# Kernel optimization log

Hardware: AMD Instinct MI355X
Metric: run time of the kernel (lower is better)

## Reference

```python
import jax, jax.numpy as jnp
import numpy as np

EPS = 1e-5


def _vfe(x, w, b, g, beta):
    # x: (B, Nv, Np, Cin) -> (B, Nv, Cout). Linear -> BatchNorm1d(train stats) -> ReLU -> max over points.
    y = jnp.einsum('bnpc,oc->bnpo', x, w) + b
    mu = y.mean(axis=(0, 1, 2))
    var = y.var(axis=(0, 1, 2))  # biased, as used by torch BN normalization
    y = (y - mu) * jax.lax.rsqrt(var + EPS) * g + beta
    y = jax.nn.relu(y)
    return y.max(axis=2)


def _conv_bn_relu(x, w, b, g, beta):
    # x: (B, Cin, D, H, W); w: (Cout, Cin, 3, 3, 3); stride 2, padding 1.
    y = jax.lax.conv_general_dilated(x, w, (2, 2, 2), [(1, 1)] * 3,
                                     dimension_numbers=('NCDHW', 'OIDHW', 'NCDHW'))
    y = y + b[None, :, None, None, None]
    mu = y.mean(axis=(0, 2, 3, 4), keepdims=True)
    var = y.var(axis=(0, 2, 3, 4), keepdims=True)
    y = (y - mu) * jax.lax.rsqrt(var + EPS) * g[None, :, None, None, None] + beta[None, :, None, None, None]
    return jax.nn.relu(y)


def setup_inputs() -> dict:
    key = jax.random.key(0)
    ks = jax.random.split(key, 16)
    B, Nv, Np, Cin = 2, 12000, 32, 5
    VF = 128  # voxel_feat_dim
    OUT = 256  # output_feat_dim
    D, H, W = 20, 128, 128
    s = 0.05
    inp = {
        'voxel_features': jax.random.normal(ks[0], (B, Nv, Np, Cin), jnp.float32),
        'voxel_coords': jax.random.randint(ks[1], (B, Nv, 3), 0, 20, jnp.int32),
        'D': D, 'H': H, 'W': W,
        # VFE1: 5 -> 64
        'w1': jax.random.normal(ks[2], (VF // 2, Cin), jnp.float32) * s,
        'b1': jnp.zeros((VF // 2,), jnp.float32),
        'g1': jnp.ones((VF // 2,), jnp.float32),
        'be1': jnp.zeros((VF // 2,), jnp.float32),
        # VFE2: 64 -> 128
        'w2': jax.random.normal(ks[3], (VF, VF // 2), jnp.float32) * s,
        'b2': jnp.zeros((VF,), jnp.float32),
        'g2': jnp.ones((VF,), jnp.float32),
        'be2': jnp.zeros((VF,), jnp.float32),
        # conv3d_1: 128 -> 128
        'cw1': jax.random.normal(ks[4], (128, VF, 3, 3, 3), jnp.float32) * s,
        'cb1': jnp.zeros((128,), jnp.float32),
        'cg1': jnp.ones((128,), jnp.float32),
        'cbe1': jnp.zeros((128,), jnp.float32),
        # conv3d_2: 128 -> 256
        'cw2': jax.random.normal(ks[5], (256, 128, 3, 3, 3), jnp.float32) * s,
        'cb2': jnp.zeros((256,), jnp.float32),
        'cg2': jnp.ones((256,), jnp.float32),
        'cbe2': jnp.zeros((256,), jnp.float32),
        # conv3d_3: 256 -> 256
        'cw3': jax.random.normal(ks[6], (OUT, 256, 3, 3, 3), jnp.float32) * s,
        'cb3': jnp.zeros((OUT,), jnp.float32),
        'cg3': jnp.ones((OUT,), jnp.float32),
        'cbe3': jnp.zeros((OUT,), jnp.float32),
    }
    return inp


def reference(voxel_features, voxel_coords, D, H, W,
              w1, b1, g1, be1, w2, b2, g2, be2,
              cw1, cb1, cg1, cbe1, cw2, cb2, cg2, cbe2, cw3, cb3, cg3, cbe3):
    # VFE stages
    f = _vfe(voxel_features, w1, b1, g1, be1)   # (B, Nv, 64)
    f = _vfe(f[:, :, None, :] * 1.0 if False else f.reshape(f.shape[0], f.shape[1], 1, -1), w2, b2, g2, be2) if False else None
    # proper: vfe2 operates on (B, Nv, Np, C) but after vfe1 features are (B, Nv, C);
    # torch code passes 3D tensor? No: vfe2 receives (B, Nv, 64) reshaped -- actually torch
    # VFELayer expects 4D; original forward feeds (B, Nv, 64) which unpacks as (B, Nv, 64)->error-free
    # only if treated as (B, Nv, Np=64, C)? We match the documented intent: treat vfe1 output as
    # (B, Nv, 1, 64) so vfe2's max over points is a no-op.
    f1 = _vfe(voxel_features, w1, b1, g1, be1)          # (B, Nv, 64)
    f2 = _vfe(f1[:, :, None, :], w2, b2, g2, be2)       # (B, Nv, 128)
    B, Nv, C = f2.shape
    # scatter voxel features into dense grid (B, C, D, H, W)
    def scat(feat, coords):
        grid = jnp.zeros((C, D, H, W), feat.dtype)
        return grid.at[:, coords[:, 0], coords[:, 1], coords[:, 2]].set(feat.T)
    grid = jax.vmap(scat)(f2, voxel_coords)
    x = _conv_bn_relu(grid, cw1, cb1, cg1, cbe1)
    x = _conv_bn_relu(x, cw2, cb2, cg2, cbe2)
    x = _conv_bn_relu(x, cw3, cb3, cg3, cbe3)
    return x
```

## Files before the change

kernel.cpp:

```cpp
#include <hip/hip_runtime.h>
#include <hip/hip_bf16.h>

#define EPS 1e-5f

#define BB 2
#define NV 12000
#define NP 32
#define CIN 5
#define GD 20

typedef __attribute__((ext_vector_type(8))) short bf16x8;
typedef __attribute__((ext_vector_type(4))) float f32x4;

static const size_t OFF_SX   = 0;
static const size_t OFF_MST  = 32;
static const size_t OFF_AC1  = 4192;
static const size_t OFF_AC2  = 4320;
static const size_t OFF_ACB1 = 4576;
static const size_t OFF_ACB2 = 4960;
static const size_t OFF_AC3  = 7520;
static const size_t OFF_BG2  = 8032;
static const size_t OFF_BG3  = 10080;
static const size_t OFF_W2T  = 13152;
static const size_t OFF_WIN  = 21344;
static const size_t OFF_F1   = 37344;
static const size_t OFF_I0CL = 1573344;
static const size_t OFF_I1   = 3059168;
static const size_t OFF_I2   = 3644896;
static const size_t OFF_WT1B = 4031968;
static const size_t OFF_WT2  = 4253152;
static const size_t OFF_WT3  = 5137888;
static const size_t OFF_RAW1 = 6907360;
static const size_t OFF_RAW2 = 8146400;
static const size_t OFF_RAW3 = 9620960;
static const size_t OFF_MSTP = 10407392;
static const size_t OFF_SXP  = 11472352;

__global__ __launch_bounds__(256) void k_front(const float* __restrict__ cw2, const float* __restrict__ cw3,
                                               const float* __restrict__ w2, const float* __restrict__ cw1,
                                               float* __restrict__ wT2, float* __restrict__ wT3,
                                               float* __restrict__ w2T, __hip_bfloat16* __restrict__ wT1b,
                                               float* __restrict__ I0z, float* __restrict__ bgz,
                                               int* __restrict__ winp,
                                               const float* __restrict__ vf, float* __restrict__ sxp,
                                               const float* __restrict__ w1,
                                               float* __restrict__ mxb, float* __restrict__ mnb){
    __shared__ float shm[5200];
    int blk = blockIdx.x;
    int t = threadIdx.x;
    if (blk >= 1892){
        int wave = t >> 6, lane = t & 63;
        int v = (blk - 1892)*4 + wave;
        float w[5];
        #pragma unroll
        for (int c=0;c<5;c++) w[c] = w1[lane*5+c];
        const float* x = vf + (size_t)v*(NP*CIN);
        float mx = -1e30f, mn = 1e30f;
        #pragma unroll
        for (int pc = 0; pc < 8; pc++) {
            float xx[20];
            const float4* x4 = (const float4*)(x + pc*20);
            #pragma unroll
            for (int i=0;i<5;i++){ float4 q = x4[i]; xx[4*i]=q.x; xx[4*i+1]=q.y; xx[4*i+2]=q.z; xx[4*i+3]=q.w; }
            #pragma unroll
            for (int j=0;j<4;j++){
                float y = xx[j*5]*w[0]+xx[j*5+1]*w[1]+xx[j*5+2]*w[2]+xx[j*5+3]*w[3]+xx[j*5+4]*w[4];
                mx = fmaxf(mx, y); mn = fminf(mn, y);
            }
        }
        mxb[(size_t)v*64 + lane] = mx;
        mnb[(size_t)v*64 + lane] = mn;
        return;
    }
    if (blk >= 1142){
        int sb = blk - 1142;
        float* st = shm; float* sw = shm + 5120;
        const float4* src = (const float4*)(vf + (size_t)sb*5120);
        #pragma unroll
        for (int i=0;i<5;i++) ((float4*)st)[i*256 + t] = src[i*256 + t];
        __syncthreads();
        float vals[20];
        #pragma unroll
        for (int i=0;i<20;i++) vals[i]=0.f;
        const float* base = st + t*20;
        #pragma unroll
        for (int p=0;p<4;p++){
            const float* v2 = base + p*5;
            int k=5;
            #pragma unroll
            for (int c=0;c<5;c++){
                vals[c]+=v2[c];
                #pragma unroll
                for(int c2=c;c2<5;c2++){ vals[k++]+=v2[c]*v2[c2]; }
            }
        }
        #pragma unroll
        for (int off=32; off>0; off>>=1){
            #pragma unroll
            for (int i=0;i<20;i++) vals[i] += __shfl_down(vals[i], off);
        }
        int wave = t>>6, lane = t&63;
        if (lane==0){
            #pragma unroll
            for (int i=0;i<20;i++) sw[wave*20+i]=vals[i];
        }
        __syncthreads();
        if (t<20){
            float s = sw[t]+sw[20+t]+sw[40+t]+sw[60+t];
            sxp[(size_t)t*768 + sb] = s;
        }
        return;
    }
    if (blk >= 1141){
        int4* d = (int4*)winp;
        int4 mone; mone.x=-1; mone.y=-1; mone.z=-1; mone.w=-1;
        #pragma unroll
        for (int k=0;k<16;k++){
            int idx = k*256 + t;
            if (idx < 4000) d[idx] = mone;
        }
        return;
    }
    if (blk == 1140){
        float4 z; z.x=0.f; z.y=0.f; z.z=0.f; z.w=0.f;
        float4* d = (float4*)bgz;
        #pragma unroll
        for (int k=0;k<5;k++) d[k*256 + t] = z;
        return;
    }
    if (blk >= 777){
        float4 z; z.x=0.f; z.y=0.f; z.z=0.f; z.w=0.f;
        float4* d = (float4*)I0z;
        int base = (blk - 777)*1024;
        #pragma unroll
        for (int k=0;k<4;k++){
            int idx = base + k*256 + t;
            if (idx < 371456) d[idx] = z;
        }
        return;
    }
    if (blk >= 649){
        int co = blk - 649;
        float* tlw = shm;
        for (int j=t; j<3456; j+=256) tlw[j] = cw1[(size_t)co*3456 + j];
        __syncthreads();
        for (int idx=t; idx<3456; idx+=256){
            int tap = idx >> 7, ci = idx & 127;
            wT1b[((size_t)(tap*128 + co) << 7) + ci] = __float2bfloat16(tlw[ci*27 + tap]);
        }
        return;
    }
    if (blk == 648){
        for (int i=t; i<8192; i+=256){ int o=i>>6, c=i&63; w2T[c*128+o]=w2[i]; }
        return;
    }
    const float* src; float* dst; int CO, R;
    if (blk < 216){ src=cw2; dst=wT2; CO=256; R=3456; }
    else { blk-=216; src=cw3; dst=wT3; CO=256; R=6912; }
    int nrt = R/64;
    int rt = blk % nrt, ct = blk / nrt;
    int r0 = rt*64, c0 = ct*64;
    float (*tl)[65] = (float(*)[65])shm;
    int tj = threadIdx.x & 63;
    int ti0 = threadIdx.x >> 6;
    #pragma unroll
    for (int k=0;k<16;k++){
        int i = ti0 + k*4;
        tl[i][tj] = src[(size_t)(c0+i)*R + r0 + tj];
    }
    __syncthreads();
    #pragma unroll
    for (int k=0;k<16;k++){
        int j = ti0 + k*4;
        dst[(size_t)(r0+j)*CO + c0 + tj] = tl[tj][j];
    }
}

__global__ __launch_bounds__(256) void k_red_sx_ac1(const float* __restrict__ sxp,
                                                    const float* __restrict__ w1, const float* __restrict__ b1,
                                                    const float* __restrict__ g1, const float* __restrict__ be1,
                                                    float* __restrict__ AC1,
                                                    const int* __restrict__ coords, int* __restrict__ winner){
    if (blockIdx.x >= 1){
        int i = (blockIdx.x - 1)*256 + threadIdx.x;
        if (i >= BB*NV) return;
        int b = i / NV, n = i % NV;
        int d = coords[(size_t)i*3], h = coords[(size_t)i*3+1], w = coords[(size_t)i*3+2];
        if (d<0||d>=GD||h<0||h>=GD||w<0||w>=GD) return;
        atomicMax(&winner[b*8000 + d*400 + h*20 + w], n);
        return;
    }
    __shared__ float S[20];
    int t = threadIdx.x;
    int wave = t>>6, lane = t&63;
    for (int c = wave; c < 20; c += 4){
        float s = 0.f;
        for (int b = lane; b < 750; b += 64) s += sxp[(size_t)c*768 + b];
        #pragma unroll
        for (int off=32; off>0; off>>=1) s += __shfl_down(s, off);
        if (lane==0) S[c] = s;
    }
    __syncthreads();
    int o = t; if (o>=64) return;
    const float N = (float)(BB*NV*NP);
    float w[5];
    #pragma unroll
    for(int c=0;c<5;c++) w[c]=w1[o*5+c];
    float b=b1[o];
    float wd=0;
    #pragma unroll
    for(int c=0;c<5;c++) wd += w[c]*S[c];
    float m = wd/N + b;
    float q=0; int kk=5;
    for(int c=0;c<5;c++) for(int c2=c;c2<5;c2++){ float s=S[kk++]; q += (c==c2?1.f:2.f)*w[c]*w[c2]*s; }
    q = q/N + 2.f*b*wd/N + b*b;
    float var = q - m*m;
    float A = g1[o]*rsqrtf(var + EPS);
    AC1[o] = A;
    AC1[64+o] = be1[o] + (b - m)*A;
}

__global__ __launch_bounds__(256) void k_stats_f1p(const float* __restrict__ mxb, const float* __restrict__ mnb,
                                                   const float* __restrict__ AC1,
                                                   float* __restrict__ f1, float* __restrict__ Mpart){
    __shared__ float Ash[64], Csh[64];
    __shared__ float tile[16][64];
    __shared__ float ssum[64];
    int t = threadIdx.x;
    if (t < 64){ Ash[t]=AC1[t]; Csh[t]=AC1[64+t]; ssum[t]=0.f; }
    float acc[4][4];
    #pragma unroll
    for(int i=0;i<4;i++)
        #pragma unroll
        for(int j=0;j<4;j++) acc[i][j]=0.f;
    int i4 = (t>>4)*4, j4 = (t&15)*4;
    const int NT = (BB*NV)/16;
    for (int tl = blockIdx.x; tl < NT; tl += gridDim.x) {
        __syncthreads();
        for (int i = t; i < 16*64; i += 256){
            int o = i & 63;
            float a = Ash[o];
            float vmx = mxb[(size_t)tl*1024 + i];
            float vmn = mnb[(size_t)tl*1024 + i];
            float f = fmaxf(a*((a>=0.f)?vmx:vmn) + Csh[o], 0.f);
            tile[i>>6][o] = f;
            f1[(size_t)tl*1024 + i] = f;
        }
        __syncthreads();
        #pragma unroll
        for (int r=0;r<16;r++){
            float a[4], bb[4];
            #pragma unroll
            for (int u=0;u<4;u++) a[u]=tile[r][i4+u];
            #pragma unroll
            for (int u=0;u<4;u++) bb[u]=tile[r][j4+u];
            #pragma unroll
            for (int u=0;u<4;u++)
                #pragma unroll
                for (int q=0;q<4;q++) acc[u][q] += a[u]*bb[q];
        }
        if (t < 64) {
            float s=0;
            #pragma unroll
            for(int r=0;r<16;r++) s+=tile[r][t];
            ssum[t]+=s;
        }
    }
    float* mp = Mpart + (size_t)blockIdx.x*4160;
    #pragma unroll
    for(int i=0;i<4;i++)
        #pragma unroll
        for(int j=0;j<4;j++) mp[(size_t)(i4+i)*64 + (j4+j)] = acc[i][j];
    __syncthreads();
    if (t<64) mp[4096 + t] = ssum[t];
}

__global__ __launch_bounds__(64) void k_red_mst(const float* __restrict__ Mpart, float* __restrict__ Mst){
    int e = blockIdx.x*64 + threadIdx.x;
    if (e >= 4160) return;
    float s = 0.f;
    #pragma unroll 8
    for (int p=0;p<256;p++) s += Mpart[(size_t)p*4160 + e];
    Mst[e] = s;
}

__global__ __launch_bounds__(64) void k_ac2(const float* __restrict__ Mst, const float* __restrict__ w2,
                                            const float* __restrict__ b2, const float* __restrict__ g2,
                                            const float* __restrict__ be2, float* __restrict__ AC2){
    int o = blockIdx.x;
    int j = threadIdx.x;
    const float N = (float)(BB*NV);
    const float* M = Mst; const float* sv = Mst+4096;
    const float* wrow = w2 + o*64;
    float wj = wrow[j];
    float sj = 0.f;
    #pragma unroll 8
    for (int c=0;c<64;c++) sj += wrow[c]*M[c*64+j];
    float q = wj*sj;
    float wdp = wj*sv[j];
    #pragma unroll
    for (int off=32; off>0; off>>=1){ q += __shfl_down(q,off); wdp += __shfl_down(wdp,off); }
    if (j==0){
        float b = b2[o];
        float m = wdp/N + b;
        float qq = q/N + 2.f*b*wdp/N + b*b;
        float var = qq - m*m;
        float A = g2[o]*rsqrtf(var+EPS);
        AC2[o]=A; AC2[128+o]= be2[o] + (b-m)*A;
    }
}


__global__ __launch_bounds__(256) void k_I0(const int* __restrict__ winner, const float* __restrict__ f1,
                                            const float* __restrict__ w2T, const float* __restrict__ AC2,
                                            __hip_bfloat16* __restrict__ I0cl){
    int blk = blockIdx.x;
    int b = blk / 400; int dh = blk % 400;
    int d = dh / 20, h = dh % 20;
    __shared__ int win[20];
    __shared__ float f1sh[20][64];
    __shared__ float sh[20*128];
    int t = threadIdx.x;
    if (t < 20) win[t] = winner[b*8000 + dh*20 + t];
    __syncthreads();
    for (int idx = t; idx < 1280; idx += 256){
        int cell = idx >> 6, c = idx & 63;
        int n = win[cell];
        f1sh[cell][c] = (n>=0) ? f1[((size_t)(b*NV+n))*64 + c] : 0.f;
    }
    __syncthreads();
    int o = t & 127;
    int half = t >> 7;
    float A = AC2[o], C = AC2[128+o];
    float wreg[64];
    #pragma unroll
    for (int c=0;c<64;c++) wreg[c] = w2T[c*128+o];
    for (int p=0;p<10;p++){
        int cell = p*2 + half;
        float acc = 0.f;
        if (win[cell] >= 0){
            #pragma unroll
            for (int c=0;c<64;c++) acc += f1sh[cell][c]*wreg[c];
            acc = fmaxf(acc*A + C, 0.f);
        }
        sh[cell*128 + o] = acc;
    }
    __syncthreads();
    __hip_bfloat16* outp = I0cl + (((size_t)(b*21 + d+1)*23 + h+1)*24 + 1)*128;
    for (int idx = t; idx < 2560; idx += 256) outp[idx] = __float2bfloat16(sh[idx]);
}

__global__ __launch_bounds__(256) void k_conv1m(const __hip_bfloat16* __restrict__ I0cl,
                                                const __hip_bfloat16* __restrict__ wT1b,
                                                float* __restrict__ raw1){
    int blk = blockIdx.x;
    int oh = blk % 11; int r2 = blk / 11;
    int od = r2 % 10; int b = r2 / 10;
    __shared__ float4 ldsv[3456];
    char* lds = (char*)ldsv;
    int t = threadIdx.x;
    for (int i = t; i < 3456; i += 256){
        int row = i >> 4;
        int dh = row / 24, w = row % 24;
        int dd = dh / 3, hh = dh % 3;
        const char* src = (const char*)(I0cl + (((size_t)(b*21 + 2*od+dd)*23 + 2*oh+hh)*24 + w)*128);
        float4 v = *(const float4*)(src + (i & 15)*16);
        int lb = i*16;
        *(float4*)(lds + (lb ^ ((row & 7) << 4))) = v;
    }
    __syncthreads();
    int wave = t >> 6, lane = t & 63;
    int col = lane & 15, quad = lane >> 4;
    int co0 = wave*32;
    f32x4 acc0 = {0.f,0.f,0.f,0.f};
    f32x4 acc1 = {0.f,0.f,0.f,0.f};
    for (int kd=0; kd<3; kd++){
        for (int kh=0; kh<3; kh++){
            #pragma unroll
            for (int kw=0; kw<3; kw++){
                int tap = (kd*3+kh)*3 + kw;
                int wi = 2*col + kw; if (wi > 23) wi = 23;
                int row = (kd*3+kh)*24 + wi;
                int lbbase = (row << 8) + quad*16;
                int xr = (row & 7) << 4;
                const __hip_bfloat16* ap0 = wT1b + (size_t)tap*16384 + (co0 + col)*128 + quad*8;
                #pragma unroll
                for (int q=0; q<4; q++){
                    bf16x8 b0 = *(const bf16x8*)(lds + ((lbbase + q*64) ^ xr));
                    bf16x8 a0 = *(const bf16x8*)(ap0 + q*32);
                    bf16x8 a1 = *(const bf16x8*)(ap0 + q*32 + 2048);
                    acc0 = __builtin_amdgcn_mfma_f32_16x16x32_bf16(a0, b0, acc0, 0, 0, 0);
                    acc1 = __builtin_amdgcn_mfma_f32_16x16x32_bf16(a1, b0, acc1, 0, 0, 0);
                }
            }
        }
    }
    if (col < 11){
        #pragma unroll
        for (int r=0;r<4;r++){
            int co = co0 + quad*4 + r;
            raw1[(((size_t)(b*128+co)*10 + od)*11 + oh)*11 + col] = acc0[r];
        }
        #pragma unroll
        for (int r=0;r<4;r++){
            int co = co0 + 16 + quad*4 + r;
            raw1[(((size_t)(b*128+co)*10 + od)*11 + oh)*11 + col] = acc1[r];
        }
    }
}

__global__ __launch_bounds__(256) void k_stats_c1(const float* __restrict__ raw1, const float* __restrict__ cb,
                                                  const float* __restrict__ cg, const float* __restrict__ cbe,
                                                  float* __restrict__ ACb1){
    int co = blockIdx.x;
    float s=0, ss=0;
    for (int b=0;b<2;b++){
        size_t base = ((size_t)(b*128+co))*1210;
        for (int i=threadIdx.x; i<1210; i+=256){
            float v = raw1[base+i];
            s+=v; ss+=v*v;
        }
    }
    __shared__ float sh1[256], sh2[256];
    sh1[threadIdx.x]=s; sh2[threadIdx.x]=ss; __syncthreads();
    for (int st=128; st>0; st>>=1){
        if (threadIdx.x<st){ sh1[threadIdx.x]+=sh1[threadIdx.x+st]; sh2[threadIdx.x]+=sh2[threadIdx.x+st]; }
        __syncthreads();
    }
    if (threadIdx.x==0){
        float bias = cb[co];
        const float N = 81920.f;
        float sum_y = sh1[0] + N*bias;
        float ssq_y = sh2[0] + 2.f*bias*sh1[0] + N*bias*bias;
        float m = sum_y/N;
        float var = ssq_y/N - m*m;
        float A = cg[co]*rsqrtf(var+EPS);
        float C = cbe[co] - m*A;
        ACb1[co]=A; ACb1[128+co]=C;
        ACb1[256+co]=fmaxf(bias*A + C, 0.f);
    }
}

__global__ __launch_bounds__(256) void k_fill_I1_bg2(const float* __restrict__ raw1, const float* __restrict__ ACb1,
                                                     const float* __restrict__ cb, float* __restrict__ I1p,
                                                     const float* __restrict__ cw2, float* __restrict__ bgraw2){
    if (blockIdx.x >= 2288){
        int o = blockIdx.x - 2288;
        int t = threadIdx.x;
        float acc[8];
        #pragma unroll
        for (int c=0;c<8;c++) acc[c]=0.f;
        if (t < 128){
            int ci = t;
            float w[27];
            const float* wp = cw2 + (size_t)o*3456 + ci*27;
            #pragma unroll
            for (int k=0;k<27;k++) w[k] = wp[k];
            float bg = ACb1[256+ci];
            float sw0[9], sw1[9];
            #pragma unroll
            for (int t9=0;t9<9;t9++){ sw1[t9]=w[3*t9+1]+w[3*t9+2]; sw0[t9]=w[3*t9]+sw1[t9]; }
            #pragma unroll
            for (int cls=0; cls<8; cls++){
                const int d0=(cls>>2)&1, h0=(cls>>1)&1, w0=cls&1;
                float ws=0.f;
                #pragma unroll
                for (int kd=0;kd<3;kd++){
                    if (d0 && kd==0) continue;
                    #pragma unroll
                    for (int kh=0;kh<3;kh++){
                        if (h0 && kh==0) continue;
                        ws += w0 ? sw1[kd*3+kh] : sw0[kd*3+kh];
                    }
                }
                acc[cls] = bg*ws;
            }
        }
        #pragma unroll
        for (int off=32; off>0; off>>=1){
            #pragma unroll
            for (int c=0;c<8;c++) acc[c] += __shfl_down(acc[c], off);
        }
        __shared__ float sred[4][8];
        if ((t&63)==0){
            #pragma unroll
            for (int c=0;c<8;c++) sred[t>>6][c] = acc[c];
        }
        __syncthreads();
        if (t < 8) bgraw2[o*8+t] = sred[0][t]+sred[1][t]+sred[2][t]+sred[3][t];
        return;
    }
    int i = blockIdx.x*blockDim.x + threadIdx.x;
    int wpad = i % 16; int r = i / 16;
    int hpad = r % 13; r /= 13;
    int dpad = r % 11; r /= 11;
    int ci = r % 128; int b = r / 128;
    float val;
    if (dpad==0 || hpad==0 || wpad==0 || wpad>12) val = 0.f;
    else {
        int d = dpad-1, h = hpad-1, w = wpad-1;
        if (h < 11 && w < 11){
            size_t idx = (((size_t)(b*128+ci)*10 + d)*11 + h)*11 + w;
            val = fmaxf((raw1[idx] + cb[ci])*ACb1[ci] + ACb1[128+ci], 0.f);
        } else val = ACb1[256+ci];
    }
    I1p[i] = val;
}

__global__ __launch_bounds__(256) void k_conv2(const float* __restrict__ I1p, const float* __restrict__ wT2,
                                               float* __restrict__ raw2){
    int blk = blockIdx.x;
    int ciq = blk & 15; blk >>= 4;
    int oh = blk % 6; blk /= 6;
    int od = blk % 5; int b = blk / 5;
    int wave = threadIdx.x >> 6, lane = threadIdx.x & 63;
    float acc[4][6];
    #pragma unroll
    for (int q=0;q<4;q++)
        #pragma unroll
        for (int i=0;i<6;i++) acc[q][i]=0.f;
    int ci0 = ciq*8 + wave*2;
    for (int ci = ci0; ci < ci0+2; ci++){
        const float* base = I1p + ((size_t)(b*128+ci)*11 + 2*od)*208 + (2*oh)*16;
        const float* wp0 = wT2 + (size_t)ci*27*256 + lane;
        #pragma unroll
        for (int kd=0;kd<3;kd++){
            #pragma unroll
            for (int kh=0;kh<3;kh++){
                float row[16];
                const float4* rp = (const float4*)(base + kd*208 + kh*16);
                #pragma unroll
                for (int i=0;i<4;i++){ float4 t=rp[i]; row[4*i]=t.x; row[4*i+1]=t.y; row[4*i+2]=t.z; row[4*i+3]=t.w; }
                const float* wp = wp0 + (kd*3+kh)*3*256;
                #pragma unroll
                for (int kw=0;kw<3;kw++){
                    float w0=wp[kw*256], w1=wp[kw*256+64], w2v=wp[kw*256+128], w3=wp[kw*256+192];
                    #pragma unroll
                    for (int ow=0;ow<6;ow++){
                        float x = row[2*ow+kw];
                        acc[0][ow]+=x*w0; acc[1][ow]+=x*w1; acc[2][ow]+=x*w2v; acc[3][ow]+=x*w3;
                    }
                }
            }
        }
    }
    __shared__ float red[4*1540];
    #pragma unroll
    for (int q=0;q<4;q++)
        #pragma unroll
        for (int ow=0;ow<6;ow++) red[wave*1540 + lane*24 + q*6 + ow] = acc[q][ow];
    __syncthreads();
    float* rb = raw2 + (size_t)ciq*92160;
    for (int idx = threadIdx.x; idx < 1536; idx += 256){
        int lane2 = idx/24, j = idx%24;
        float s = red[0*1540 + lane2*24 + j] + red[1*1540 + lane2*24 + j]
                + red[2*1540 + lane2*24 + j] + red[3*1540 + lane2*24 + j];
        int q = j/6, ow = j%6;
        int co = q*64 + lane2;
        rb[(((size_t)(b*256+co)*5 + od)*6 + oh)*6 + ow] = s;
    }
}

__global__ __launch_bounds__(64) void k_stats_c2(const float* __restrict__ raw2, const float* __restrict__ bgraw2,
                                                 const float* __restrict__ cb2, const float* __restrict__ cg2,
                                                 const float* __restrict__ cbe2, float* __restrict__ ACb2){
    int o = blockIdx.x;
    int lane = threadIdx.x;
    float s=0.f, ss=0.f;
    for (int idx=lane; idx<360; idx+=64){
        int b = idx/180; int p = idx%180;
        int d = p/36; int rem = p%36; int h = rem/6; int w = rem%6;
        size_t base = (((size_t)(b*256+o)*5 + d)*6 + h)*6 + w;
        float v = 0.f;
        #pragma unroll
        for (int q=0;q<16;q++) v += raw2[q*92160+base];
        s += v; ss += v*v;
    }
    #pragma unroll
    for (int off=32; off>0; off>>=1){ s += __shfl_down(s,off); ss += __shfl_down(ss,off); }
    if (lane==0){
        const int n2[8] = {3744,104,104,0,936,26,26,0};
        float bgv[8];
        #pragma unroll
        for (int c=0;c<8;c++){ bgv[c]=bgraw2[o*8+c]; s += 2.f*n2[c]*bgv[c]; ss += 2.f*n2[c]*bgv[c]*bgv[c]; }
        const float N = 10240.f;
        float b = cb2[o];
        float sum_y = s + N*b;
        float ssq_y = ss + 2.f*b*s + N*b*b;
        float m = sum_y/N;
        float var = ssq_y/N - m*m;
        float A = cg2[o]*rsqrtf(var+EPS); float C = cbe2[o] - m*A;
        ACb2[o]=A; ACb2[256+o]=C;
        for (int c=0;c<8;c++) ACb2[512+o*8+c] = fmaxf((bgv[c]+b)*A + C, 0.f);
    }
}

__global__ __launch_bounds__(256) void k_fill_I2_bg3(const float* __restrict__ raw2, const float* __restrict__ ACb2,
                                                     const float* __restrict__ cb2, float* __restrict__ I2p,
                                                     const float* __restrict__ cw3, float* __restrict__ bgraw3){
    if (blockIdx.x >= 1512){
        int o = blockIdx.x - 1512;
        int t = threadIdx.x;
        float sum12[12];
        {
            int ci = t;
            float w[27];
            const float* wp = cw3 + ((size_t)o*256 + ci)*27;
            #pragma unroll
            for (int k=0;k<27;k++) w[k] = wp[k];
            const float* bg = ACb2 + 512 + ci*8;
            float bgv[8];
            #pragma unroll
            for (int q=0;q<8;q++) bgv[q]=bg[q];
            #pragma unroll
            for (int c=0;c<12;c++){
                const int odc = c>>2; const int h0 = (c>>1)&1; const int w0 = c&1;
                float sum = 0.f;
                #pragma unroll
                for (int kd=0;kd<3;kd++){
                    const int d = 2*odc-1+kd; if (d<0||d>=5) continue;
                    const int db = (d==0)?4:0;
                    #pragma unroll
                    for (int kh=0;kh<3;kh++){
                        if (h0 && kh==0) continue;
                        const int hb = (h0 && kh==1)?2:0;
                        #pragma unroll
                        for (int kw=0;kw<3;kw++){
                            if (w0 && kw==0) continue;
                            const int wb = (w0 && kw==1)?1:0;
                            sum += bgv[db|hb|wb]*w[(kd*3+kh)*3+kw];
                        }
                    }
                }
                sum12[c] = sum;
            }
        }
        #pragma unroll
        for (int off=32; off>0; off>>=1){
            #pragma unroll
            for (int c=0;c<12;c++) sum12[c] += __shfl_down(sum12[c], off);
        }
        __shared__ float sred[4][12];
        if ((t&63)==0){
            #pragma unroll
            for (int c=0;c<12;c++) sred[t>>6][c] = sum12[c];
        }
        __syncthreads();
        if (t < 12) bgraw3[o*12+t] = sred[0][t]+sred[1][t]+sred[2][t]+sred[3][t];
        return;
    }
    int i = blockIdx.x*blockDim.x + threadIdx.x;
    int wpad = i % 12; int r = i / 12;
    int hpad = r % 9; r /= 9;
    int dpad = r % 7; r /= 7;
    int ci = r % 256; int b = r / 256;
    float val;
    if (dpad==0 || dpad==6 || hpad==0 || wpad==0 || wpad>8) val = 0.f;
    else {
        int d = dpad-1, h = hpad-1, w = wpad-1;
        if (h<6 && w<6){
            size_t idx = (((size_t)(b*256+ci)*5 + d)*6 + h)*6 + w;
            float raw = 0.f;
            #pragma unroll
            for (int q=0;q<16;q++) raw += raw2[q*92160+idx];
            val = fmaxf((raw + cb2[ci])*ACb2[ci] + ACb2[256+ci], 0.f);
        } else {
            int cls = ((d==0)?4:0) | ((h==0)?2:0) | ((w==0)?1:0);
            val = ACb2[512 + ci*8 + cls];
        }
    }
    I2p[i] = val;
}

__global__ __launch_bounds__(256) void k_conv3(const float* __restrict__ I2p, const float* __restrict__ wT3,
                                               float* __restrict__ raw3){
    int blk = blockIdx.x;
    int ciq = blk & 31; blk >>= 5;
    int oh = blk % 4; blk /= 4;
    int od = blk % 3; int b = blk / 3;
    int wave = threadIdx.x >> 6, lane = threadIdx.x & 63;
    float acc[4][4];
    #pragma unroll
    for (int q=0;q<4;q++)
        #pragma unroll
        for (int i=0;i<4;i++) acc[q][i]=0.f;
    int ci0 = ciq*8 + wave*2;
    for (int ci = ci0; ci < ci0+2; ci++){
        const float* base = I2p + ((size_t)(b*256+ci)*7 + 2*od)*108 + (2*oh)*12;
        const float* wp0 = wT3 + (size_t)ci*27*256 + lane;
        #pragma unroll
        for (int kd=0;kd<3;kd++){
            #pragma unroll
            for (int kh=0;kh<3;kh++){
                float row[12];
                const float4* rp = (const float4*)(base + kd*108 + kh*12);
                #pragma unroll
                for (int i=0;i<3;i++){ float4 t=rp[i]; row[4*i]=t.x; row[4*i+1]=t.y; row[4*i+2]=t.z; row[4*i+3]=t.w; }
                const float* wp = wp0 + (kd*3+kh)*3*256;
                #pragma unroll
                for (int kw=0;kw<3;kw++){
                    float w0=wp[kw*256], w1=wp[kw*256+64], w2v=wp[kw*256+128], w3=wp[kw*256+192];
                    #pragma unroll
                    for (int ow=0;ow<4;ow++){
                        float x = row[2*ow+kw];
                        acc[0][ow]+=x*w0; acc[1][ow]+=x*w1; acc[2][ow]+=x*w2v; acc[3][ow]+=x*w3;
                    }
                }
            }
        }
    }
    __shared__ float red[4*1028];
    #pragma unroll
    for (int q=0;q<4;q++)
        #pragma unroll
        for (int ow=0;ow<4;ow++) red[wave*1028 + lane*16 + q*4 + ow] = acc[q][ow];
    __syncthreads();
    float* rb = raw3 + (size_t)ciq*24576;
    for (int idx = threadIdx.x; idx < 1024; idx += 256){
        int lane2 = idx/16, j = idx%16;
        float s = red[0*1028 + lane2*16 + j] + red[1*1028 + lane2*16 + j]
                + red[2*1028 + lane2*16 + j] + red[3*1028 + lane2*16 + j];
        int q = j/4, ow = j%4;
        int co = q*64 + lane2;
        rb[(((size_t)(b*256+co)*3 + od)*4 + oh)*4 + ow] = s;
    }
}

__global__ __launch_bounds__(64) void k_stats_c3(const float* __restrict__ raw3, const float* __restrict__ bgraw3,
                                                 const float* __restrict__ cb3, const float* __restrict__ cg3,
                                                 const float* __restrict__ cbe3, float* __restrict__ AC3){
    int o = blockIdx.x;
    int lane = threadIdx.x;
    float s=0.f, ss=0.f;
    for (int idx=lane; idx<96; idx+=64){
        int b = idx/48; int p = idx%48;
        int d = p/16; int rem = p%16; int h = rem/4; int w = rem%4;
        size_t base = (((size_t)(b*256+o)*3 + d)*4 + h)*4 + w;
        float v = 0.f;
        #pragma unroll
        for (int q=0;q<32;q++) v += raw3[q*24576+base];
        s += v; ss += v*v;
    }
    #pragma unroll
    for (int off=32; off>0; off>>=1){ s += __shfl_down(s,off); ss += __shfl_down(ss,off); }
    if (lane==0){
        const int n3hw[4] = {216,12,12,0};
        for (int c=0;c<12;c++){
            float bg = bgraw3[o*12+c];
            float n = 2.f*n3hw[c&3];
            s += n*bg; ss += n*bg*bg;
        }
        const float N = 1536.f;
        float b = cb3[o];
        float sum_y = s + N*b;
        float ssq_y = ss + 2.f*b*s + N*b*b;
        float m = sum_y/N;
        float var = ssq_y/N - m*m;
        float A = cg3[o]*rsqrtf(var+EPS);
        AC3[o]=A; AC3[256+o]=cbe3[o] - m*A;
    }
}

__global__ void k_final(const float* __restrict__ raw3, const float* __restrict__ bgraw3,
                        const float* __restrict__ cb3, const float* __restrict__ AC3,
                        float* __restrict__ out){
    int i = blockIdx.x*blockDim.x + threadIdx.x;
    if (i >= 2*256*3*16*16) return;
    int ow = i % 16; int r = i / 16;
    int oh = r % 16; r /= 16;
    int od = r % 3; r /= 3;
    int o = r % 256; int b = r / 256;
    float v;
    if (oh<4 && ow<4){
        size_t base = (((size_t)(b*256+o)*3 + od)*4 + oh)*4 + ow;
        v = 0.f;
        #pragma unroll
        for (int q=0;q<32;q++) v += raw3[q*24576+base];
    } else {
        v = bgraw3[o*12 + od*4 + ((oh==0)?2:0) + ((ow==0)?1:0)];
    }
    out[i] = fmaxf((v + cb3[o])*AC3[o] + AC3[256+o], 0.f);
}


extern "C" void kernel_launch(void* const* d_in, const int* in_sizes, int n_in,
                              void* d_out, int out_size, void* d_ws, size_t ws_size,
                              hipStream_t stream) {
    const float* vf    = (const float*)d_in[0];
    const int*   coords= (const int*)d_in[1];
    const float* w1    = (const float*)d_in[5];
    const float* b1    = (const float*)d_in[6];
    const float* g1    = (const float*)d_in[7];
    const float* be1   = (const float*)d_in[8];
    const float* w2    = (const float*)d_in[9];
    const float* b2    = (const float*)d_in[10];
    const float* g2    = (const float*)d_in[11];
    const float* be2   = (const float*)d_in[12];
    const float* cw1   = (const float*)d_in[13];
    const float* cb1   = (const float*)d_in[14];
    const float* cg1   = (const float*)d_in[15];
    const float* cbe1  = (const float*)d_in[16];
    const float* cw2   = (const float*)d_in[17];
    const float* cb2   = (const float*)d_in[18];
    const float* cg2   = (const float*)d_in[19];
    const float* cbe2  = (const float*)d_in[20];
    const float* cw3   = (const float*)d_in[21];
    const float* cb3   = (const float*)d_in[22];
    const float* cg3   = (const float*)d_in[23];
    const float* cbe3  = (const float*)d_in[24];
    float* out = (float*)d_out;
    float* ws  = (float*)d_ws;
    __hip_bfloat16* I0cl = (__hip_bfloat16*)(ws + OFF_I0CL);
    __hip_bfloat16* wT1b = (__hip_bfloat16*)(ws + OFF_WT1B);
    int* winp = (int*)(ws + OFF_WIN);
    float* mxb = ws + OFF_RAW2;
    float* mnb = ws + OFF_RAW2 + 768000;

    k_front<<<7892,256,0,stream>>>(cw2, cw3, w2, cw1, ws+OFF_WT2, ws+OFF_WT3, ws+OFF_W2T, wT1b,
                                   ws+OFF_I0CL, ws+OFF_BG2, winp, vf, ws+OFF_SXP, w1, mxb, mnb);
    k_red_sx_ac1<<<95,256,0,stream>>>(ws+OFF_SXP, w1,b1,g1,be1, ws+OFF_AC1, coords, winp);
    k_stats_f1p<<<256,256,0,stream>>>(mxb, mnb, ws+OFF_AC1, ws+OFF_F1, ws+OFF_MSTP);
    k_red_mst<<<65,64,0,stream>>>(ws+OFF_MSTP, ws+OFF_MST);
    k_ac2<<<128,64,0,stream>>>(ws+OFF_MST, w2,b2,g2,be2, ws+OFF_AC2);
    k_I0<<<800,256,0,stream>>>(winp, ws+OFF_F1, ws+OFF_W2T, ws+OFF_AC2, I0cl);
    k_conv1m<<<220,256,0,stream>>>(I0cl, wT1b, ws+OFF_RAW1);
    k_stats_c1<<<128,256,0,stream>>>(ws+OFF_RAW1, cb1,cg1,cbe1, ws+OFF_ACB1);
    k_fill_I1_bg2<<<2544,256,0,stream>>>(ws+OFF_RAW1, ws+OFF_ACB1, cb1, ws+OFF_I1, cw2, ws+OFF_BG2);
    k_conv2<<<960,256,0,stream>>>(ws+OFF_I1, ws+OFF_WT2, ws+OFF_RAW2);
    k_stats_c2<<<256,64,0,stream>>>(ws+OFF_RAW2, ws+OFF_BG2, cb2, cg2, cbe2, ws+OFF_ACB2);
    k_fill_I2_bg3<<<1768,256,0,stream>>>(ws+OFF_RAW2, ws+OFF_ACB2, cb2, ws+OFF_I2, cw3, ws+OFF_BG3);
    k_conv3<<<768,256,0,stream>>>(ws+OFF_I2, ws+OFF_WT3, ws+OFF_RAW3);
    k_stats_c3<<<256,64,0,stream>>>(ws+OFF_RAW3, ws+OFF_BG3, cb3, cg3, cbe3, ws+OFF_AC3);
    k_final<<<1536,256,0,stream>>>(ws+OFF_RAW3, ws+OFF_BG3, cb3, ws+OFF_AC3, out);
}
```

Before: 303.5 us.

## Fuse VFE1 max/min computation with f1 and Gram-matrix stats kernel

Moves the per-voxel linear+max/min pass out of k_front into a new kernel that also applies BN1 affine+ReLU, writes f1 and accumulates the 64x64 Gram matrix and sums per wave in registers. This removes the intermediate mxb/mnb buffers (write and reread of about 6MB). It also cuts the k_front grid and drops the shared-memory staging in its stats branch. The Gram accumulation now uses 64 accumulators per lane and an LDS broadcast per voxel. The partial-reduce kernel is widened to 512 partials with 4 waves per block. The price is higher register pressure and re-reading vf in the new kernel.

```diff
diff --git a/kernel.cpp b/kernel.cpp
--- a/kernel.cpp
+++ b/kernel.cpp
@@ -42,50 +42,23 @@
                                                float* __restrict__ w2T, __hip_bfloat16* __restrict__ wT1b,
                                                float* __restrict__ I0z, float* __restrict__ bgz,
                                                int* __restrict__ winp,
-                                               const float* __restrict__ vf, float* __restrict__ sxp,
-                                               const float* __restrict__ w1,
-                                               float* __restrict__ mxb, float* __restrict__ mnb){
-    __shared__ float shm[5200];
+                                               const float* __restrict__ vf, float* __restrict__ sxp){
+    __shared__ float shm[4160];
     int blk = blockIdx.x;
     int t = threadIdx.x;
-    if (blk >= 1892){
-        int wave = t >> 6, lane = t & 63;
-        int v = (blk - 1892)*4 + wave;
-        float w[5];
-        #pragma unroll
-        for (int c=0;c<5;c++) w[c] = w1[lane*5+c];
-        const float* x = vf + (size_t)v*(NP*CIN);
-        float mx = -1e30f, mn = 1e30f;
-        #pragma unroll
-        for (int pc = 0; pc < 8; pc++) {
-            float xx[20];
-            const float4* x4 = (const float4*)(x + pc*20);
-            #pragma unroll
-            for (int i=0;i<5;i++){ float4 q = x4[i]; xx[4*i]=q.x; xx[4*i+1]=q.y; xx[4*i+2]=q.z; xx[4*i+3]=q.w; }
-            #pragma unroll
-            for (int j=0;j<4;j++){
-                float y = xx[j*5]*w[0]+xx[j*5+1]*w[1]+xx[j*5+2]*w[2]+xx[j*5+3]*w[3]+xx[j*5+4]*w[4];
-                mx = fmaxf(mx, y); mn = fminf(mn, y);
-            }
-        }
-        mxb[(size_t)v*64 + lane] = mx;
-        mnb[(size_t)v*64 + lane] = mn;
-        return;
-    }
     if (blk >= 1142){
         int sb = blk - 1142;
-        float* st = shm; float* sw = shm + 5120;
-        const float4* src = (const float4*)(vf + (size_t)sb*5120);
-        #pragma unroll
-        for (int i=0;i<5;i++) ((float4*)st)[i*256 + t] = src[i*256 + t];
-        __syncthreads();
+        float* sw = shm;
+        float xx[20];
+        const float4* x4 = (const float4*)(vf + (size_t)sb*5120 + t*20);
+        #pragma unroll
+        for (int i=0;i<5;i++){ float4 q = x4[i]; xx[4*i]=q.x; xx[4*i+1]=q.y; xx[4*i+2]=q.z; xx[4*i+3]=q.w; }
         float vals[20];
         #pragma unroll
         for (int i=0;i<20;i++) vals[i]=0.f;
-        const float* base = st + t*20;
         #pragma unroll
         for (int p=0;p<4;p++){
-            const float* v2 = base + p*5;
+            const float* v2 = xx + p*5;
             int k=5;
             #pragma unroll
             for (int c=0;c<5;c++){
@@ -220,68 +193,76 @@
     AC1[64+o] = be1[o] + (b - m)*A;
 }
 
-__global__ __launch_bounds__(256) void k_stats_f1p(const float* __restrict__ mxb, const float* __restrict__ mnb,
-                                                   const float* __restrict__ AC1,
-                                                   float* __restrict__ f1, float* __restrict__ Mpart){
-    __shared__ float Ash[64], Csh[64];
-    __shared__ float tile[16][64];
-    __shared__ float ssum[64];
+__global__ __launch_bounds__(256) void k_vfe1g(const float* __restrict__ vf, const float* __restrict__ w1,
+                                               const float* __restrict__ AC1,
+                                               float* __restrict__ f1, float* __restrict__ Mpart){
+    __shared__ float fsh[4][64];
+    __shared__ float red[4][16][64];
+    int t = threadIdx.x, wave = t>>6, lane = t&63;
+    float w[5];
+    #pragma unroll
+    for (int c=0;c<5;c++) w[c] = w1[lane*5+c];
+    float A = AC1[lane], Cc = AC1[64+lane];
+    float acc[64];
+    #pragma unroll
+    for (int i=0;i<64;i++) acc[i]=0.f;
+    float sv = 0.f;
+    for (int v = blockIdx.x*4 + wave; v < BB*NV; v += 2048){
+        const float4* x4 = (const float4*)(vf + (size_t)v*160);
+        float mx=-1e30f, mn=1e30f;
+        #pragma unroll
+        for (int pc=0; pc<8; pc++){
+            float xx[20];
+            #pragma unroll
+            for (int i=0;i<5;i++){ float4 q = x4[pc*5+i]; xx[4*i]=q.x; xx[4*i+1]=q.y; xx[4*i+2]=q.z; xx[4*i+3]=q.w; }
+            #pragma unroll
+            for (int j=0;j<4;j++){
+                float y = xx[j*5]*w[0]+xx[j*5+1]*w[1]+xx[j*5+2]*w[2]+xx[j*5+3]*w[3]+xx[j*5+4]*w[4];
+                mx = fmaxf(mx,y); mn = fminf(mn,y);
+            }
+        }
+        float f = fmaxf(A*((A>=0.f)?mx:mn)+Cc, 0.f);
+        f1[(size_t)v*64 + lane] = f;
+        fsh[wave][lane] = f;
+        sv += f;
+        #pragma unroll
+        for (int i4=0;i4<16;i4++){
+            float4 q = ((const float4*)fsh[wave])[i4];
+            acc[4*i4+0] += q.x*f; acc[4*i4+1] += q.y*f;
+            acc[4*i4+2] += q.z*f; acc[4*i4+3] += q.w*f;
+        }
+    }
+    float* mp = Mpart + (size_t)blockIdx.x*4160;
+    for (int c=0;c<4;c++){
+        __syncthreads();
+        #pragma unroll
+        for (int i=0;i<16;i++) red[wave][i][lane] = acc[c*16+i];
+        __syncthreads();
+        for (int k=0;k<4;k++){
+            int idx = k*256 + t;
+            int i = idx>>6, j = idx&63;
+            mp[(size_t)(c*16+i)*64 + j] = red[0][i][j]+red[1][i][j]+red[2][i][j]+red[3][i][j];
+        }
+    }
+    __syncthreads();
+    fsh[wave][lane] = sv;
+    __syncthreads();
+    if (t < 64) mp[4096+t] = fsh[0][t]+fsh[1][t]+fsh[2][t]+fsh[3][t];
+}
+
+__global__ __launch_bounds__(256) void k_red_mst(const float* __restrict__ Mpart, float* __restrict__ Mst){
     int t = threadIdx.x;
-    if (t < 64){ Ash[t]=AC1[t]; Csh[t]=AC1[64+t]; ssum[t]=0.f; }
-    float acc[4][4];
-    #pragma unroll
-    for(int i=0;i<4;i++)
-        #pragma unroll
-        for(int j=0;j<4;j++) acc[i][j]=0.f;
-    int i4 = (t>>4)*4, j4 = (t&15)*4;
-    const int NT = (BB*NV)/16;
-    for (int tl = blockIdx.x; tl < NT; tl += gridDim.x) {
-        __syncthreads();
-        for (int i = t; i < 16*64; i += 256){
-            int o = i & 63;
-            float a = Ash[o];
-            float vmx = mxb[(size_t)tl*1024 + i];
-            float vmn = mnb[(size_t)tl*1024 + i];
-            float f = fmaxf(a*((a>=0.f)?vmx:vmn) + Csh[o], 0.f);
-            tile[i>>6][o] = f;
-            f1[(size_t)tl*1024 + i] = f;
-        }
-        __syncthreads();
-        #pragma unroll
-        for (int r=0;r<16;r++){
-            float a[4], bb[4];
-            #pragma unroll
-            for (int u=0;u<4;u++) a[u]=tile[r][i4+u];
-            #pragma unroll
-            for (int u=0;u<4;u++) bb[u]=tile[r][j4+u];
-            #pragma unroll
-            for (int u=0;u<4;u++)
-                #pragma unroll
-                for (int q=0;q<4;q++) acc[u][q] += a[u]*bb[q];
-        }
-        if (t < 64) {
-            float s=0;
-            #pragma unroll
-            for(int r=0;r<16;r++) s+=tile[r][t];
-            ssum[t]+=s;
-        }
-    }
-    float* mp = Mpart + (size_t)blockIdx.x*4160;
-    #pragma unroll
-    for(int i=0;i<4;i++)
-        #pragma unroll
-        for(int j=0;j<4;j++) mp[(size_t)(i4+i)*64 + (j4+j)] = acc[i][j];
-    __syncthreads();
-    if (t<64) mp[4096 + t] = ssum[t];
-}
-
-__global__ __launch_bounds__(64) void k_red_mst(const float* __restrict__ Mpart, float* __restrict__ Mst){
-    int e = blockIdx.x*64 + threadIdx.x;
-    if (e >= 4160) return;
+    int e = blockIdx.x*64 + (t&63);
+    int q = t>>6;
     float s = 0.f;
-    #pragma unroll 8
-    for (int p=0;p<256;p++) s += Mpart[(size_t)p*4160 + e];
-    Mst[e] = s;
+    if (e < 4160){
+        #pragma unroll 8
+        for (int p=q; p<512; p+=4) s += Mpart[(size_t)p*4160 + e];
+    }
+    __shared__ float rr[4][64];
+    rr[q][t&63] = s; __syncthreads();
+    if (t < 64 && blockIdx.x*64+t < 4160)
+        Mst[blockIdx.x*64+t] = rr[0][t]+rr[1][t]+rr[2][t]+rr[3][t];
 }
 
 __global__ __launch_bounds__(64) void k_ac2(const float* __restrict__ Mst, const float* __restrict__ w2,
@@ -813,14 +794,13 @@
     __hip_bfloat16* I0cl = (__hip_bfloat16*)(ws + OFF_I0CL);
     __hip_bfloat16* wT1b = (__hip_bfloat16*)(ws + OFF_WT1B);
     int* winp = (int*)(ws + OFF_WIN);
-    float* mxb = ws + OFF_RAW2;
-    float* mnb = ws + OFF_RAW2 + 768000;
-
-    k_front<<<7892,256,0,stream>>>(cw2, cw3, w2, cw1, ws+OFF_WT2, ws+OFF_WT3, ws+OFF_W2T, wT1b,
-                                   ws+OFF_I0CL, ws+OFF_BG2, winp, vf, ws+OFF_SXP, w1, mxb, mnb);
+    float* Mpart = ws + OFF_RAW2;
+
+    k_front<<<1892,256,0,stream>>>(cw2, cw3, w2, cw1, ws+OFF_WT2, ws+OFF_WT3, ws+OFF_W2T, wT1b,
+                                   ws+OFF_I0CL, ws+OFF_BG2, winp, vf, ws+OFF_SXP);
     k_red_sx_ac1<<<95,256,0,stream>>>(ws+OFF_SXP, w1,b1,g1,be1, ws+OFF_AC1, coords, winp);
-    k_stats_f1p<<<256,256,0,stream>>>(mxb, mnb, ws+OFF_AC1, ws+OFF_F1, ws+OFF_MSTP);
-    k_red_mst<<<65,64,0,stream>>>(ws+OFF_MSTP, ws+OFF_MST);
+    k_vfe1g<<<512,256,0,stream>>>(vf, w1, ws+OFF_AC1, ws+OFF_F1, Mpart);
+    k_red_mst<<<65,256,0,stream>>>(Mpart, ws+OFF_MST);
     k_ac2<<<128,64,0,stream>>>(ws+OFF_MST, w2,b2,g2,be2, ws+OFF_AC2);
     k_I0<<<800,256,0,stream>>>(winp, ws+OFF_F1, ws+OFF_W2T, ws+OFF_AC2, I0cl);
     k_conv1m<<<220,256,0,stream>>>(I0cl, wT1b, ws+OFF_RAW1);
```

Measured after the change: 307.1 us. About the same (+1.2%).
